# Optimization experiments

Measured on AMD Instinct MI355X. Metric: run time of the kernel, lower is better.

Reference implementation:

```python
import jax, jax.numpy as jnp
import numpy as np

TEMPERATURE = 0.5
EPS = 1e-8
NEG = -1e30  # effectively -inf for masked logits


def _l2norm(x):
    n = jnp.sqrt(jnp.sum(x * x, axis=1, keepdims=True))
    return x / jnp.maximum(n, EPS)


def setup_inputs() -> dict:
    key = jax.random.key(0)
    ks = jax.random.split(key, 4)
    N, D = 2048, 128
    return {f"projection_image_aug{i+1}": jax.random.normal(ks[i], (N, D), dtype=jnp.float32)
            for i in range(4)}


def reference(projection_image_aug1, projection_image_aug2,
              projection_image_aug3, projection_image_aug4):
    zs = [projection_image_aug1.astype(jnp.float32),
          projection_image_aug2.astype(jnp.float32),
          projection_image_aug3.astype(jnp.float32),
          projection_image_aug4.astype(jnp.float32)]
    N = zs[0].shape[0]
    k = len(zs)
    z = jnp.concatenate(zs[:2], axis=0)        # [2N, D]
    z_all = jnp.concatenate(zs, axis=0)        # [kN, D]
    # cosine sim via normalize + matmul (same math as broadcast CosineSimilarity)
    sim = _l2norm(z) @ _l2norm(z_all).T / TEMPERATURE   # [2N, kN]

    rows = jnp.arange(2 * N)
    half = rows // N                 # 0 for first N rows, 1 for second
    idx = rows % N
    cols = jnp.arange(k * N)
    block = cols // N
    # mask: diagonal entries of every N-block except the target block (1-half)
    diag = (cols[None, :] % N) == idx[:, None]
    mask = diag & (block[None, :] != (1 - half)[:, None])
    sim_m = jnp.where(mask, NEG, sim)
    # positive column: aug2 partner for rows<N, aug1 partner for rows>=N
    target_col = (1 - half) * N + idx
    pos = jnp.take_along_axis(sim_m, target_col[:, None], axis=1)[:, 0]
    # cross_entropy(reduction='sum') / (2N)
    loss = jnp.sum(jax.nn.logsumexp(sim_m, axis=1) - pos) / (2 * N)
    return loss
```

## Files before the change

kernel.cpp:

```cpp
#include <hip/hip_runtime.h>
#include <hip/hip_bf16.h>


#define NN      2048
#define DD      128
#define TWO_N   4096
#define FOUR_N  8192
#define CTG     16
#define SQRT_C  1.6986436f
#define LN2     0.6931471805599453f

using frag_ab = __attribute__((ext_vector_type(8))) short;
using f32x4   = __attribute__((ext_vector_type(4))) float;

__global__ __launch_bounds__(256) void knorm(const float* __restrict__ p0,
                                             const float* __restrict__ p1,
                                             const float* __restrict__ p2,
                                             const float* __restrict__ p3,
                                             short* __restrict__ Bn,
                                             float* __restrict__ out) {
  if (blockIdx.x == 0 && threadIdx.x == 0) out[0] = 0.0f;
  int wave = threadIdx.x >> 6, lane = threadIdx.x & 63;
  int row = blockIdx.x * 4 + wave;
  int q = row >> 11, idx = row & (NN - 1);
  const float* src = (q == 0) ? p0 : (q == 1) ? p1 : (q == 2) ? p2 : p3;
  const float2* s2 = (const float2*)(src + (size_t)idx * DD);
  float2 v = s2[lane];
  float ss = v.x * v.x + v.y * v.y;
  #pragma unroll
  for (int sh = 1; sh < 64; sh <<= 1) ss += __shfl_xor(ss, sh, 64);
  float inv = SQRT_C / fmaxf(sqrtf(ss), 1e-8f);
  __hip_bfloat162 o;
  o.x = __float2bfloat16(v.x * inv);
  o.y = __float2bfloat16(v.y * inv);
  ((__hip_bfloat162*)(Bn + (size_t)row * DD))[lane] = o;
}

__global__ __launch_bounds__(1024, 4) void kgemm(const short* __restrict__ Bn,
                                                 float* __restrict__ pS) {
  __shared__ float sS[256][5];

  int t = threadIdx.x, wave = t >> 6, lane = t & 63;
  int quad = lane >> 4, l16 = lane & 15;
  int rowH = wave >> 2, colO = wave & 3;

  int lin = blockIdx.x;
  int by = (lin & 7) | ((lin >> 7) << 3);
  int bx = (lin >> 3) & 15;

  const short* gA = Bn + (size_t)(bx * 256 + rowH * 64 + l16) * DD + quad * 8;
  frag_ab a[4][4];
  #pragma unroll
  for (int rf = 0; rf < 4; ++rf)
    #pragma unroll
    for (int k = 0; k < 4; ++k)
      a[k][rf] = *(const frag_ab*)(gA + (size_t)rf * 16 * DD + k * 32);

  const short* gB = Bn + (size_t)(by * 512 + colO * 16 + l16) * DD + quad * 8;

  float sAcc[4][4];
  #pragma unroll
  for (int rf = 0; rf < 4; ++rf)
    #pragma unroll
    for (int r = 0; r < 4; ++r) sAcc[rf][r] = 0.f;

  frag_ab bb[4];
  #pragma unroll
  for (int k = 0; k < 4; ++k)
    bb[k] = *(const frag_ab*)(gB + k * 32);

  #pragma unroll 1
  for (int g = 0; g < 8; ++g) {
    f32x4 acc[4];
    #pragma unroll
    for (int rf = 0; rf < 4; ++rf) acc[rf] = (f32x4){0.f, 0.f, 0.f, 0.f};

    __builtin_amdgcn_s_setprio(1);
    #pragma unroll
    for (int k = 0; k < 4; ++k)
      #pragma unroll
      for (int rf = 0; rf < 4; ++rf)
        acc[rf] = __builtin_amdgcn_mfma_f32_16x16x32_bf16(a[k][rf], bb[k], acc[rf], 0, 0, 0);
    __builtin_amdgcn_s_setprio(0);

    if (g < 7) {
      const short* gBn = gB + (size_t)(g + 1) * 64 * DD;
      #pragma unroll
      for (int k = 0; k < 4; ++k)
        bb[k] = *(const frag_ab*)(gBn + k * 32);
    }
    __builtin_amdgcn_sched_barrier(0);

    #pragma unroll
    for (int rf = 0; rf < 4; ++rf)
      #pragma unroll
      for (int r = 0; r < 4; ++r)
        sAcc[rf][r] += __builtin_amdgcn_exp2f(acc[rf][r]);
  }

  #pragma unroll
  for (int rf = 0; rf < 4; ++rf)
    #pragma unroll
    for (int r = 0; r < 4; ++r) {
      float s = sAcc[rf][r];
      s += __shfl_xor(s, 1, 64);
      s += __shfl_xor(s, 2, 64);
      s += __shfl_xor(s, 4, 64);
      s += __shfl_xor(s, 8, 64);
      if (l16 == 0) sS[rowH * 64 + rf * 16 + quad * 4 + r][colO] = s;
    }
  __syncthreads();
  if (t < 256)
    pS[(size_t)(bx * 256 + t) * CTG + by] =
        (sS[t][0] + sS[t][1]) + (sS[t][2] + sS[t][3]);
}

__global__ __launch_bounds__(256) void kfin(const short* __restrict__ Bn,
                                            const float* __restrict__ pS,
                                            float* __restrict__ out) {
  int t = threadIdx.x, wave = t >> 6, lane = t & 63;
  int grBase = blockIdx.x * 16;
  __shared__ float sRed[4];

  float wloss = 0.f;
  #pragma unroll 1
  for (int rr = wave; rr < 16; rr += 4) {
    int gr = grBase + rr;
    int idx = gr & (NN - 1), half = gr >> 11;
    float S = (lane < CTG) ? pS[(size_t)gr * CTG + lane] : 0.f;
    #pragma unroll
    for (int sh = 1; sh < 16; sh <<= 1) S += __shfl_xor(S, sh, 64);
    unsigned int ua = ((const unsigned int*)(Bn + (size_t)gr * DD))[lane];
    unsigned int ub = ((const unsigned int*)(Bn + (size_t)((1 - half) * NN + idx) * DD))[lane];
    unsigned int uc = ((const unsigned int*)(Bn + (size_t)(2 * NN + idx) * DD))[lane];
    unsigned int ud = ((const unsigned int*)(Bn + (size_t)(3 * NN + idx) * DD))[lane];
    float a0 = __uint_as_float((ua & 0xffffu) << 16), a1 = __uint_as_float(ua & 0xffff0000u);
    float b0 = __uint_as_float((ub & 0xffffu) << 16), b1 = __uint_as_float(ub & 0xffff0000u);
    float c0 = __uint_as_float((uc & 0xffffu) << 16), c1 = __uint_as_float(uc & 0xffff0000u);
    float d0 = __uint_as_float((ud & 0xffffu) << 16), d1 = __uint_as_float(ud & 0xffff0000u);
    float daa = a0 * a0 + a1 * a1;
    float dab = a0 * b0 + a1 * b1;
    float dac = a0 * c0 + a1 * c1;
    float dad = a0 * d0 + a1 * d1;
    #pragma unroll
    for (int sh = 1; sh < 64; sh <<= 1) {
      daa += __shfl_xor(daa, sh, 64);
      dab += __shfl_xor(dab, sh, 64);
      dac += __shfl_xor(dac, sh, 64);
      dad += __shfl_xor(dad, sh, 64);
    }
    float Sc = S - __builtin_amdgcn_exp2f(daa)
                 - __builtin_amdgcn_exp2f(dac)
                 - __builtin_amdgcn_exp2f(dad);
    float loss = LN2 * (__log2f(Sc) - dab);
    if (lane == 0) wloss += loss;
  }
  if (lane == 0) sRed[wave] = wloss;
  __syncthreads();
  if (t == 0)
    atomicAdd(out, (sRed[0] + sRed[1] + sRed[2] + sRed[3]) * (1.0f / (float)TWO_N));
}

extern "C" void kernel_launch(void* const* d_in, const int* in_sizes, int n_in,
                              void* d_out, int out_size, void* d_ws, size_t ws_size,
                              hipStream_t stream) {
  (void)in_sizes; (void)n_in; (void)out_size; (void)ws_size;
  const float* p0 = (const float*)d_in[0];
  const float* p1 = (const float*)d_in[1];
  const float* p2 = (const float*)d_in[2];
  const float* p3 = (const float*)d_in[3];

  short* Bn = (short*)d_ws;
  float* pS = (float*)((char*)d_ws + (size_t)FOUR_N * DD * sizeof(short));
  float* out = (float*)d_out;

  knorm<<<FOUR_N / 4, 256, 0, stream>>>(p0, p1, p2, p3, Bn, out);
  kgemm<<<256, 1024, 0, stream>>>(Bn, pS);
  kfin<<<TWO_N / 16, 256, 0, stream>>>(Bn, pS, out);
}
```

Measured before the change: 96.63 us.

## Fuse normalize, GEMM and finalize into one cooperative kernel with grid syncs

Merges the three launches (row normalization, the bf16 MFMA similarity/exp-sum kernel, and the per-row loss finalize) into a single cooperative kernel of 256 blocks of 1024 threads. Phases are separated by grid-wide synchronizations instead of kernel boundaries. The normalize phase now uses float4 loads with half-wave row reductions. The aim is to remove inter-kernel launch gaps and tail effects, at the cost of two grid barriers, cooperative-launch overhead, and requiring all 256 blocks to be co-resident.

```diff
diff --git a/kernel.cpp b/kernel.cpp
--- a/kernel.cpp
+++ b/kernel.cpp
@@ -1,5 +1,8 @@
 #include <hip/hip_runtime.h>
 #include <hip/hip_bf16.h>
+#include <hip/hip_cooperative_groups.h>
+
+namespace cg = cooperative_groups;
 
 
 #define NN      2048
@@ -13,119 +16,113 @@
 using frag_ab = __attribute__((ext_vector_type(8))) short;
 using f32x4   = __attribute__((ext_vector_type(4))) float;
 
-__global__ __launch_bounds__(256) void knorm(const float* __restrict__ p0,
-                                             const float* __restrict__ p1,
-                                             const float* __restrict__ p2,
-                                             const float* __restrict__ p3,
-                                             short* __restrict__ Bn,
-                                             float* __restrict__ out) {
-  if (blockIdx.x == 0 && threadIdx.x == 0) out[0] = 0.0f;
-  int wave = threadIdx.x >> 6, lane = threadIdx.x & 63;
-  int row = blockIdx.x * 4 + wave;
-  int q = row >> 11, idx = row & (NN - 1);
-  const float* src = (q == 0) ? p0 : (q == 1) ? p1 : (q == 2) ? p2 : p3;
-  const float2* s2 = (const float2*)(src + (size_t)idx * DD);
-  float2 v = s2[lane];
-  float ss = v.x * v.x + v.y * v.y;
-  #pragma unroll
-  for (int sh = 1; sh < 64; sh <<= 1) ss += __shfl_xor(ss, sh, 64);
-  float inv = SQRT_C / fmaxf(sqrtf(ss), 1e-8f);
-  __hip_bfloat162 o;
-  o.x = __float2bfloat16(v.x * inv);
-  o.y = __float2bfloat16(v.y * inv);
-  ((__hip_bfloat162*)(Bn + (size_t)row * DD))[lane] = o;
-}
-
-__global__ __launch_bounds__(1024, 4) void kgemm(const short* __restrict__ Bn,
-                                                 float* __restrict__ pS) {
+__global__ __launch_bounds__(1024, 4) void kfused(
+    const float* __restrict__ p0, const float* __restrict__ p1,
+    const float* __restrict__ p2, const float* __restrict__ p3,
+    short* __restrict__ Bn, float* __restrict__ pS, float* __restrict__ out) {
+  cg::grid_group grid = cg::this_grid();
   __shared__ float sS[256][5];
 
   int t = threadIdx.x, wave = t >> 6, lane = t & 63;
   int quad = lane >> 4, l16 = lane & 15;
-  int rowH = wave >> 2, colO = wave & 3;
 
-  int lin = blockIdx.x;
-  int by = (lin & 7) | ((lin >> 7) << 3);
-  int bx = (lin >> 3) & 15;
+  if (blockIdx.x == 0 && t == 0) out[0] = 0.0f;
+  {
+    int l32 = lane & 31;
+    int row = blockIdx.x * 32 + wave * 2 + (lane >> 5);
+    int q = row >> 11, idx = row & (NN - 1);
+    const float* src = (q == 0) ? p0 : (q == 1) ? p1 : (q == 2) ? p2 : p3;
+    float4 v = ((const float4*)(src + (size_t)idx * DD))[l32];
+    float ss = v.x * v.x + v.y * v.y + v.z * v.z + v.w * v.w;
+    #pragma unroll
+    for (int sh = 1; sh < 32; sh <<= 1) ss += __shfl_xor(ss, sh, 64);
+    float inv = SQRT_C / fmaxf(sqrtf(ss), 1e-8f);
+    __hip_bfloat162 h0, h1;
+    h0.x = __float2bfloat16(v.x * inv); h0.y = __float2bfloat16(v.y * inv);
+    h1.x = __float2bfloat16(v.z * inv); h1.y = __float2bfloat16(v.w * inv);
+    uint2 u;
+    u.x = *(unsigned int*)&h0;
+    u.y = *(unsigned int*)&h1;
+    *(uint2*)(Bn + (size_t)row * DD + l32 * 4) = u;
+  }
+  grid.sync();
 
-  const short* gA = Bn + (size_t)(bx * 256 + rowH * 64 + l16) * DD + quad * 8;
-  frag_ab a[4][4];
-  #pragma unroll
-  for (int rf = 0; rf < 4; ++rf)
+  {
+    int rowH = wave >> 2, colO = wave & 3;
+    int lin = blockIdx.x;
+    int by = (lin & 7) | ((lin >> 7) << 3);
+    int bx = (lin >> 3) & 15;
+
+    const short* gA = Bn + (size_t)(bx * 256 + rowH * 64 + l16) * DD + quad * 8;
+    frag_ab a[4][4];
+    #pragma unroll
+    for (int rf = 0; rf < 4; ++rf)
+      #pragma unroll
+      for (int k = 0; k < 4; ++k)
+        a[k][rf] = *(const frag_ab*)(gA + (size_t)rf * 16 * DD + k * 32);
+
+    const short* gB = Bn + (size_t)(by * 512 + colO * 16 + l16) * DD + quad * 8;
+
+    float sAcc[4][4];
+    #pragma unroll
+    for (int rf = 0; rf < 4; ++rf)
+      #pragma unroll
+      for (int r = 0; r < 4; ++r) sAcc[rf][r] = 0.f;
+
+    frag_ab bb[4];
     #pragma unroll
     for (int k = 0; k < 4; ++k)
-      a[k][rf] = *(const frag_ab*)(gA + (size_t)rf * 16 * DD + k * 32);
+      bb[k] = *(const frag_ab*)(gB + k * 32);
 
-  const short* gB = Bn + (size_t)(by * 512 + colO * 16 + l16) * DD + quad * 8;
+    #pragma unroll 1
+    for (int g = 0; g < 8; ++g) {
+      f32x4 acc[4];
+      #pragma unroll
+      for (int rf = 0; rf < 4; ++rf) acc[rf] = (f32x4){0.f, 0.f, 0.f, 0.f};
 
-  float sAcc[4][4];
-  #pragma unroll
-  for (int rf = 0; rf < 4; ++rf)
-    #pragma unroll
-    for (int r = 0; r < 4; ++r) sAcc[rf][r] = 0.f;
+      __builtin_amdgcn_s_setprio(1);
+      #pragma unroll
+      for (int k = 0; k < 4; ++k)
+        #pragma unroll
+        for (int rf = 0; rf < 4; ++rf)
+          acc[rf] = __builtin_amdgcn_mfma_f32_16x16x32_bf16(a[k][rf], bb[k], acc[rf], 0, 0, 0);
+      __builtin_amdgcn_s_setprio(0);
 
-  frag_ab bb[4];
-  #pragma unroll
-  for (int k = 0; k < 4; ++k)
-    bb[k] = *(const frag_ab*)(gB + k * 32);
+      if (g < 7) {
+        const short* gBn = gB + (size_t)(g + 1) * 64 * DD;
+        #pragma unroll
+        for (int k = 0; k < 4; ++k)
+          bb[k] = *(const frag_ab*)(gBn + k * 32);
+      }
+      __builtin_amdgcn_sched_barrier(0);
 
-  #pragma unroll 1
-  for (int g = 0; g < 8; ++g) {
-    f32x4 acc[4];
-    #pragma unroll
-    for (int rf = 0; rf < 4; ++rf) acc[rf] = (f32x4){0.f, 0.f, 0.f, 0.f};
-
-    __builtin_amdgcn_s_setprio(1);
-    #pragma unroll
-    for (int k = 0; k < 4; ++k)
       #pragma unroll
       for (int rf = 0; rf < 4; ++rf)
-        acc[rf] = __builtin_amdgcn_mfma_f32_16x16x32_bf16(a[k][rf], bb[k], acc[rf], 0, 0, 0);
-    __builtin_amdgcn_s_setprio(0);
-
-    if (g < 7) {
-      const short* gBn = gB + (size_t)(g + 1) * 64 * DD;
-      #pragma unroll
-      for (int k = 0; k < 4; ++k)
-        bb[k] = *(const frag_ab*)(gBn + k * 32);
+        #pragma unroll
+        for (int r = 0; r < 4; ++r)
+          sAcc[rf][r] += __builtin_amdgcn_exp2f(acc[rf][r]);
     }
-    __builtin_amdgcn_sched_barrier(0);
 
     #pragma unroll
     for (int rf = 0; rf < 4; ++rf)
       #pragma unroll
-      for (int r = 0; r < 4; ++r)
-        sAcc[rf][r] += __builtin_amdgcn_exp2f(acc[rf][r]);
+      for (int r = 0; r < 4; ++r) {
+        float s = sAcc[rf][r];
+        s += __shfl_xor(s, 1, 64);
+        s += __shfl_xor(s, 2, 64);
+        s += __shfl_xor(s, 4, 64);
+        s += __shfl_xor(s, 8, 64);
+        if (l16 == 0) sS[rowH * 64 + rf * 16 + quad * 4 + r][colO] = s;
+      }
+    __syncthreads();
+    if (t < 256)
+      pS[(size_t)(bx * 256 + t) * CTG + by] =
+          (sS[t][0] + sS[t][1]) + (sS[t][2] + sS[t][3]);
   }
+  grid.sync();
 
-  #pragma unroll
-  for (int rf = 0; rf < 4; ++rf)
-    #pragma unroll
-    for (int r = 0; r < 4; ++r) {
-      float s = sAcc[rf][r];
-      s += __shfl_xor(s, 1, 64);
-      s += __shfl_xor(s, 2, 64);
-      s += __shfl_xor(s, 4, 64);
-      s += __shfl_xor(s, 8, 64);
-      if (l16 == 0) sS[rowH * 64 + rf * 16 + quad * 4 + r][colO] = s;
-    }
-  __syncthreads();
-  if (t < 256)
-    pS[(size_t)(bx * 256 + t) * CTG + by] =
-        (sS[t][0] + sS[t][1]) + (sS[t][2] + sS[t][3]);
-}
-
-__global__ __launch_bounds__(256) void kfin(const short* __restrict__ Bn,
-                                            const float* __restrict__ pS,
-                                            float* __restrict__ out) {
-  int t = threadIdx.x, wave = t >> 6, lane = t & 63;
-  int grBase = blockIdx.x * 16;
-  __shared__ float sRed[4];
-
-  float wloss = 0.f;
-  #pragma unroll 1
-  for (int rr = wave; rr < 16; rr += 4) {
-    int gr = grBase + rr;
+  {
+    int gr = blockIdx.x * 16 + wave;
     int idx = gr & (NN - 1), half = gr >> 11;
     float S = (lane < CTG) ? pS[(size_t)gr * CTG + lane] : 0.f;
     #pragma unroll
@@ -153,12 +150,15 @@
                  - __builtin_amdgcn_exp2f(dac)
                  - __builtin_amdgcn_exp2f(dad);
     float loss = LN2 * (__log2f(Sc) - dab);
-    if (lane == 0) wloss += loss;
+    if (lane == 0) sS[wave][0] = loss;
+    __syncthreads();
+    if (t == 0) {
+      float acc = 0.f;
+      #pragma unroll
+      for (int w = 0; w < 16; ++w) acc += sS[w][0];
+      atomicAdd(out, acc * (1.0f / (float)TWO_N));
+    }
   }
-  if (lane == 0) sRed[wave] = wloss;
-  __syncthreads();
-  if (t == 0)
-    atomicAdd(out, (sRed[0] + sRed[1] + sRed[2] + sRed[3]) * (1.0f / (float)TWO_N));
 }
 
 extern "C" void kernel_launch(void* const* d_in, const int* in_sizes, int n_in,
@@ -174,7 +174,7 @@
   float* pS = (float*)((char*)d_ws + (size_t)FOUR_N * DD * sizeof(short));
   float* out = (float*)d_out;
 
-  knorm<<<FOUR_N / 4, 256, 0, stream>>>(p0, p1, p2, p3, Bn, out);
-  kgemm<<<256, 1024, 0, stream>>>(Bn, pS);
-  kfin<<<TWO_N / 16, 256, 0, stream>>>(Bn, pS, out);
+  void* args[] = {(void*)&p0, (void*)&p1, (void*)&p2, (void*)&p3,
+                  (void*)&Bn, (void*)&pS, (void*)&out};
+  hipLaunchCooperativeKernel((void*)kfused, dim3(256), dim3(1024), args, 0, stream);
 }
```

Result: slower. 165.6 us (+71.4%).
